# Kernel optimization log

Hardware: AMD Instinct MI355X
Metric: run time of the kernel (lower is better)

## Reference

```python
import jax, jax.numpy as jnp
import numpy as np

H = 512
W = 512
N_STROKES = 5000
S = 10          # samples_per_curve
K = 20          # strokes_per_pixel
CANVAS_COLOR = 0.5  # 'gray'
COARSE = 5      # coarse grid downsample factor (H//5, W//5)


def setup_inputs() -> dict:
    key = jax.random.key(0)
    ks = jax.random.split(key, 6)
    # stroke centers spread over the canvas
    location = jax.random.uniform(ks[0], (N_STROKES, 2), jnp.float32) * jnp.array([H, W], jnp.float32)
    # bezier control-point offsets relative to the stroke center
    curve_s = jax.random.normal(ks[1], (N_STROKES, 2), jnp.float32) * 8.0
    curve_e = jax.random.normal(ks[2], (N_STROKES, 2), jnp.float32) * 8.0
    curve_c = jax.random.normal(ks[3], (N_STROKES, 2), jnp.float32) * 8.0
    color = jax.random.uniform(ks[4], (N_STROKES, 3), jnp.float32)
    width = jax.random.uniform(ks[5], (N_STROKES, 1), jnp.float32) * 4.0 + 1.0
    return {"curve_s": curve_s, "curve_e": curve_e, "curve_c": curve_c,
            "color": color, "location": location, "width": width}


def _bezier_points(s, c, e, num_points):
    # s, c, e: [N, 2] -> [N, num_points, 2]
    t = jnp.linspace(0.0, 1.0, num_points).astype(jnp.float32)  # [S]
    omt2 = (1.0 - t) ** 2  # [S]
    t2 = t ** 2
    # x/y computed identically: c + (1-t)^2 (s - c) + t^2 (e - c)
    pts = c[:, None, :] + omt2[None, :, None] * (s - c)[:, None, :] \
          + t2[None, :, None] * (e - c)[:, None, :]
    return pts  # [N, S, 2]


def _nearest_upsample_idx(out_size, in_size):
    # torch F.interpolate mode='nearest': src = floor(dst * in/out)
    idx = jnp.floor(jnp.arange(out_size) * (in_size / out_size)).astype(jnp.int32)
    return jnp.clip(idx, 0, in_size - 1)


def reference(curve_s, curve_e, curve_c, color, location, width):
    # sample bezier curve points (absolute coords)
    pts = _bezier_points(curve_s + location, curve_c + location,
                         curve_e + location, S)  # [N, S, 2]

    # ---- coarse-grid KNN over stroke centers ----
    Hc, Wc = H // COARSE, W // COARSE
    tH = jnp.linspace(0.0, float(H), Hc).astype(jnp.float32)
    tW = jnp.linspace(0.0, float(W), Wc).astype(jnp.float32)
    Px, Py = jnp.meshgrid(tH, tW, indexing='ij')
    P = jnp.stack([Px, Py], axis=-1)  # [Hc, Wc, 2]
    D_centers = jnp.sum(jnp.square(P[:, :, None, :] - location), axis=-1)  # [Hc, Wc, N]
    _, idcs = jax.lax.top_k(-D_centers, K)  # [Hc, Wc, K]

    near_pts = pts[idcs]      # [Hc, Wc, K, S, 2]
    near_col = color[idcs]    # [Hc, Wc, K, 3]
    near_w = width[idcs]      # [Hc, Wc, K, 1]

    # ---- upsample coarse gathers to full res ----
    ih = _nearest_upsample_idx(H, Hc)
    iw = _nearest_upsample_idx(W, Wc)
    near_pts = near_pts[ih][:, iw]   # [H, W, K, S, 2] (nearest)
    near_col = near_col[ih][:, iw]   # [H, W, K, 3]   (nearest)
    # widths: bilinear (align_corners=False, no antialias) per channel
    near_w = jax.image.resize(near_w[..., 0], (H, W, K), method='linear')[..., None]  # [H, W, K, 1]

    # ---- full-res pixel grid ----
    tHf = jnp.linspace(0.0, float(H), H).astype(jnp.float32)
    tWf = jnp.linspace(0.0, float(W), W).astype(jnp.float32)
    Pxf, Pyf = jnp.meshgrid(tHf, tWf, indexing='ij')
    P_full = jnp.stack([Pxf, Pyf], axis=-1)  # [H, W, 2]

    # ---- per-pixel closest point on each polyline segment ----
    a = near_pts[:, :, :, :S - 1, :]              # [H, W, K, S-1, 2]
    b_a = near_pts[:, :, :, 1:, :] - a            # segment direction
    pa = P_full[:, :, None, None, :] - a          # pixel - segment start
    t = jnp.sum(b_a * pa, axis=-1) / jnp.sum(jnp.square(b_a), axis=-1)
    t = jnp.clip(t, 0.0, 1.0)
    closest = a + t[..., None] * b_a
    dist = jnp.sum(jnp.square(P_full[:, :, None, None, :] - closest), axis=-1)  # [H, W, K, S-1]

    D = jnp.min(dist, axis=(-1, -2))  # [H, W]
    min_per_stroke = jnp.min(dist, axis=-1)  # [H, W, K]
    ranking = jax.nn.softmax(100000.0 * (1.0 / (1e-08 + min_per_stroke)), axis=-1)  # [H, W, K]

    I_colors = jnp.einsum('hwkf,hwk->hwf', near_col, ranking)  # [H, W, 3]
    bs = jnp.einsum('hwkf,hwk->hwf', near_w, ranking)          # [H, W, 1]
    bs_mask = jax.nn.sigmoid(bs - D[..., None])
    canvas = jnp.full_like(I_colors, CANVAS_COLOR)
    I = I_colors * bs_mask + (1.0 - bs_mask) * canvas
    return I
```

## Files before the change

kernel.cpp:

```cpp
#include <hip/hip_runtime.h>
#include <math.h>

#define NS 5000
#define SS 10
#define KK 20
#define HC 102
#define NBIN 32
#define BINW 16.0f
#define CAP 192

#define WAVE_SYNC() __asm__ volatile("s_waitcnt lgkmcnt(0)" ::: "memory")

__global__ void prep_kernel(const float* __restrict__ cs, const float* __restrict__ ce,
                            const float* __restrict__ cc, const float* __restrict__ loc,
                            float* __restrict__ pts, float* __restrict__ invs,
                            int* __restrict__ binCnt) {
    int i = blockIdx.x * 256 + threadIdx.x;
    if (i >= NS) return;
    float lx = loc[i*2+0], ly = loc[i*2+1];
    float sx = cs[i*2+0] + lx, sy = cs[i*2+1] + ly;
    float ex = ce[i*2+0] + lx, ey = ce[i*2+1] + ly;
    float px = cc[i*2+0] + lx, py = cc[i*2+1] + ly;
    float qx[SS], qy[SS];
    #pragma unroll
    for (int j = 0; j < SS; ++j) {
        float t = (float)j * (1.0f / 9.0f);
        float omt = 1.0f - t;
        float omt2 = omt * omt, t2 = t * t;
        qx[j] = px + omt2 * (sx - px) + t2 * (ex - px);
        qy[j] = py + omt2 * (sy - py) + t2 * (ey - py);
        pts[(i*SS+j)*2+0] = qx[j];
        pts[(i*SS+j)*2+1] = qy[j];
    }
    #pragma unroll
    for (int sg = 0; sg < 9; ++sg) {
        float bx = qx[sg+1] - qx[sg], by = qy[sg+1] - qy[sg];
        invs[i*12+sg] = 1.0f / (bx*bx + by*by);
    }
    invs[i*12+9] = 0.0f; invs[i*12+10] = 0.0f; invs[i*12+11] = 0.0f;
    int b0 = min(max((int)(lx * (1.0f/BINW)), 0), NBIN-1);
    int b1 = min(max((int)(ly * (1.0f/BINW)), 0), NBIN-1);
    atomicAdd(&binCnt[b0*NBIN + b1], 1);
}

__global__ void binscan_kernel(const int* __restrict__ binCnt, int* __restrict__ binStart) {
    __shared__ int tmp[NBIN*NBIN];
    int t = threadIdx.x;
    tmp[t] = binCnt[t];
    __syncthreads();
    for (int off = 1; off < NBIN*NBIN; off <<= 1) {
        int v = (t >= off) ? tmp[t - off] : 0;
        __syncthreads();
        tmp[t] += v;
        __syncthreads();
    }
    binStart[t + 1] = tmp[t];
    if (t == 0) binStart[0] = 0;
}

__global__ void binscatter_kernel(const float* __restrict__ loc, const int* __restrict__ binStart,
                                  int* __restrict__ binFill, float2* __restrict__ sxy,
                                  int* __restrict__ sid) {
    int i = blockIdx.x * 256 + threadIdx.x;
    if (i >= NS) return;
    float l0 = loc[i*2+0], l1 = loc[i*2+1];
    int b0 = min(max((int)(l0 * (1.0f/BINW)), 0), NBIN-1);
    int b1 = min(max((int)(l1 * (1.0f/BINW)), 0), NBIN-1);
    int b = b0*NBIN + b1;
    int pos = binStart[b] + atomicAdd(&binFill[b], 1);
    sxy[pos] = make_float2(l0, l1);
    sid[pos] = i;
}

__global__ void __launch_bounds__(256) topk_kernel(const float* __restrict__ loc,
                                                   const float* __restrict__ width,
                                                   const float2* __restrict__ sxy,
                                                   const int* __restrict__ sid,
                                                   const int* __restrict__ binStart,
                                                   int* __restrict__ idcs,
                                                   float* __restrict__ wk) {
    __shared__ unsigned long long sk[4][CAP];
    int w = threadIdx.x >> 6, lane = threadIdx.x & 63;
    int cell = blockIdx.x * 4 + w;
    int ci = cell / HC, cj = cell - ci * HC;
    const float dc = 512.0f / 101.0f;
    float c0 = (float)ci * dc;
    float c1 = (float)cj * dc;
    unsigned long long below = (1ull << lane) - 1ull;

    float R = 30.0f;
    int cnt = 0;
    for (int attempt = 0; attempt < 5; ++attempt) {
        float R2 = R * R;
        int base = 0;
        int by0 = max((int)((c0 - R) * (1.0f/BINW)), 0);
        int by1 = min((int)((c0 + R) * (1.0f/BINW)), NBIN-1);
        int bx0 = max((int)((c1 - R) * (1.0f/BINW)), 0);
        int bx1 = min((int)((c1 + R) * (1.0f/BINW)), NBIN-1);
        for (int by = by0; by <= by1; ++by) {
            int s = binStart[by*NBIN + bx0];
            int e = binStart[by*NBIN + bx1 + 1];
            for (int t0 = s; t0 < e; t0 += 64) {
                int t = t0 + lane;
                int tc = min(t, e - 1);
                float2 p = sxy[tc];
                float dx = c0 - p.x, dy = c1 - p.y;
                float d = dx*dx + dy*dy;
                bool pred = (t < e) && (d < R2);
                unsigned long long mask = __ballot(pred);
                int pos = base + __popcll(mask & below);
                if (pred && pos < CAP)
                    sk[w][pos] = ((unsigned long long)__float_as_uint(d) << 32)
                               | (unsigned int)sid[tc];
                base += __popcll(mask);
            }
        }
        cnt = base;
        if (cnt >= KK) break;
        R *= 1.6f;
    }
    WAVE_SYNC();

    if (cnt >= KK && cnt <= CAP) {
        if (cnt <= 64) {
            unsigned long long k0 = (lane < cnt) ? sk[w][lane] : ~0ull;
            int r0 = 0;
            int j = 0;
            #pragma unroll 1
            for (; j + 4 <= cnt; j += 4) {
                unsigned long long a = sk[w][j],   b = sk[w][j+1];
                unsigned long long c = sk[w][j+2], d = sk[w][j+3];
                r0 += (int)(a < k0) + (int)(b < k0) + (int)(c < k0) + (int)(d < k0);
            }
            for (; j < cnt; ++j) r0 += (int)(sk[w][j] < k0);
            if (r0 < KK && lane < cnt) {
                int idx = (int)(unsigned int)(k0 & 0xffffffffull);
                idcs[cell*KK + r0] = idx;
                wk[cell*KK + r0]   = width[idx];
            }
        } else {
            unsigned long long k0 = (lane       < cnt) ? sk[w][lane]       : ~0ull;
            unsigned long long k1 = (lane + 64  < cnt) ? sk[w][lane + 64]  : ~0ull;
            unsigned long long k2 = (lane + 128 < cnt) ? sk[w][lane + 128] : ~0ull;
            int r0 = 0, r1 = 0, r2 = 0;
            #pragma unroll 1
            for (int j = 0; j < cnt; ++j) {
                unsigned long long a = sk[w][j];
                r0 += (int)(a < k0); r1 += (int)(a < k1); r2 += (int)(a < k2);
            }
            if (r0 < KK && lane < cnt) {
                int idx = (int)(unsigned int)(k0 & 0xffffffffull);
                idcs[cell*KK + r0] = idx;  wk[cell*KK + r0] = width[idx];
            }
            if (r1 < KK && lane + 64 < cnt) {
                int idx = (int)(unsigned int)(k1 & 0xffffffffull);
                idcs[cell*KK + r1] = idx;  wk[cell*KK + r1] = width[idx];
            }
            if (r2 < KK && lane + 128 < cnt) {
                int idx = (int)(unsigned int)(k2 & 0xffffffffull);
                idcs[cell*KK + r2] = idx;  wk[cell*KK + r2] = width[idx];
            }
        }
    } else {
        if (lane == 0) {
            float bd[KK]; int bi[KK];
            for (int k = 0; k < KK; ++k) { bd[k] = 3.4e38f; bi[k] = 0; }
            for (int n = 0; n < NS; ++n) {
                float dx = c0 - loc[n*2+0];
                float dy = c1 - loc[n*2+1];
                float d = dx*dx + dy*dy;
                if (d < bd[KK-1]) {
                    int p = KK - 1;
                    while (p > 0 && bd[p-1] > d) { bd[p] = bd[p-1]; bi[p] = bi[p-1]; --p; }
                    bd[p] = d; bi[p] = n;
                }
            }
            for (int k = 0; k < KK; ++k) {
                idcs[cell*KK + k] = bi[k];
                wk[cell*KK + k]   = width[bi[k]];
            }
        }
    }
}

__global__ void __launch_bounds__(256) render_kernel(const float* __restrict__ pts,
                                                     const float* __restrict__ invs,
                                                     const float* __restrict__ color,
                                                     const int* __restrict__ idcs,
                                                     const float* __restrict__ wk,
                                                     float* __restrict__ out) {
    int x = blockIdx.x * 64 + threadIdx.x;
    int y = blockIdx.y * 4  + threadIdx.y;
    const float df = 512.0f / 511.0f;
    float p0 = (float)y * df;
    float p1 = (float)x * df;
    int cy = (y * 51) >> 8;
    int cx = (x * 51) >> 8;
    const int* mi = idcs + (cy * HC + cx) * KK;

    const float sc = 102.0f / 512.0f;
    float iny = ((float)y + 0.5f) * sc - 0.5f;
    float inx = ((float)x + 0.5f) * sc - 0.5f;
    float y0f = floorf(iny), x0f = floorf(inx);
    float fy = iny - y0f, fx = inx - x0f;
    int y0 = min(max((int)y0f, 0), HC - 1);
    int y1 = min(max((int)y0f + 1, 0), HC - 1);
    int x0 = min(max((int)x0f, 0), HC - 1);
    int x1 = min(max((int)x0f + 1, 0), HC - 1);
    const float* w00 = wk + (y0 * HC + x0) * KK;
    const float* w01 = wk + (y0 * HC + x1) * KK;
    const float* w10 = wk + (y1 * HC + x0) * KK;
    const float* w11 = wk + (y1 * HC + x1) * KK;

    float m = -INFINITY, s = 0.0f;
    float a0 = 0.0f, a1 = 0.0f, a2 = 0.0f, wa = 0.0f;
    float D = INFINITY;

    #pragma unroll 1
    for (int k = 0; k < KK; ++k) {
        int idx = mi[k];
        const float4* pf = (const float4*)(pts  + idx * 20);
        const float4* vf = (const float4*)(invs + idx * 12);
        float4 f0 = pf[0], f1 = pf[1], f2 = pf[2], f3 = pf[3], f4 = pf[4];
        float4 i0 = vf[0], i1 = vf[1], i2 = vf[2];
        float qx[10] = {f0.x, f0.z, f1.x, f1.z, f2.x, f2.z, f3.x, f3.z, f4.x, f4.z};
        float qy[10] = {f0.y, f0.w, f1.y, f1.w, f2.y, f2.w, f3.y, f3.w, f4.y, f4.w};
        float iv[9]  = {i0.x, i0.y, i0.z, i0.w, i1.x, i1.y, i1.z, i1.w, i2.x};
        float mink = INFINITY;
        #pragma unroll
        for (int sg = 0; sg < 9; ++sg) {
            float ax = qx[sg], ay = qy[sg];
            float bx = qx[sg+1] - ax, by = qy[sg+1] - ay;
            float pax = p0 - ax, pay = p1 - ay;
            float dot = bx * pax + by * pay;
            float t = dot * iv[sg];
            t = fminf(fmaxf(t, 0.0f), 1.0f);
            float ccx = ax + t * bx, ccy = ay + t * by;
            float ddx = p0 - ccx, ddy = p1 - ccy;
            float d = ddx * ddx + ddy * ddy;
            mink = fminf(mink, d);
        }
        D = fminf(D, mink);
        float xk = 100000.0f / (1e-8f + mink);
        float wkv = (1.0f - fy) * ((1.0f - fx) * w00[k] + fx * w01[k])
                  +          fy * ((1.0f - fx) * w10[k] + fx * w11[k]);
        float c0v = color[idx*3+0], c1v = color[idx*3+1], c2v = color[idx*3+2];
        if (xk > m) {
            float scl = __expf(m - xk);
            s  = s  * scl + 1.0f;
            a0 = a0 * scl + c0v;
            a1 = a1 * scl + c1v;
            a2 = a2 * scl + c2v;
            wa = wa * scl + wkv;
            m = xk;
        } else {
            float e = __expf(xk - m);
            s  += e;
            a0 += c0v * e;
            a1 += c1v * e;
            a2 += c2v * e;
            wa += wkv * e;
        }
    }
    float inv = 1.0f / s;
    float bs = wa * inv;
    float msk = 1.0f / (1.0f + __expf(-(bs - D)));
    float o0 = a0 * inv * msk + (1.0f - msk) * 0.5f;
    float o1 = a1 * inv * msk + (1.0f - msk) * 0.5f;
    float o2 = a2 * inv * msk + (1.0f - msk) * 0.5f;
    int base = (y * 512 + x) * 3;
    out[base+0] = o0;
    out[base+1] = o1;
    out[base+2] = o2;
}

extern "C" void kernel_launch(void* const* d_in, const int* in_sizes, int n_in,
                              void* d_out, int out_size, void* d_ws, size_t ws_size,
                              hipStream_t stream) {
    const float* cs    = (const float*)d_in[0];
    const float* ce    = (const float*)d_in[1];
    const float* cc    = (const float*)d_in[2];
    const float* color = (const float*)d_in[3];
    const float* loc   = (const float*)d_in[4];
    const float* width = (const float*)d_in[5];
    float* out = (float*)d_out;

    char* p = (char*)d_ws;
    float*  pts      = (float*)p;                 p += NS * SS * 2 * sizeof(float);
    float*  invs     = (float*)p;                 p += NS * 12 * sizeof(float);
    int*    idcs     = (int*)p;                   p += (size_t)HC*HC*KK*sizeof(int);
    float*  wk       = (float*)p;                 p += (size_t)HC*HC*KK*sizeof(float);
    int*    binCnt   = (int*)p;                   p += NBIN*NBIN*sizeof(int);
    int*    binFill  = (int*)p;                   p += NBIN*NBIN*sizeof(int);
    int*    binStart = (int*)p;                   p += 4112;
    float2* sxy      = (float2*)p;                p += NS * sizeof(float2);
    int*    sid      = (int*)p;

    hipMemsetAsync(binCnt, 0, 2 * NBIN * NBIN * sizeof(int), stream);

    prep_kernel      <<<(NS + 255) / 256, 256, 0, stream>>>(cs, ce, cc, loc, pts, invs, binCnt);
    binscan_kernel   <<<1, NBIN*NBIN, 0, stream>>>(binCnt, binStart);
    binscatter_kernel<<<(NS + 255) / 256, 256, 0, stream>>>(loc, binStart, binFill, sxy, sid);
    topk_kernel      <<<(HC*HC)/4, 256, 0, stream>>>(loc, width, sxy, sid, binStart, idcs, wk);
    render_kernel    <<<dim3(512/64, 512/4), dim3(64, 4), 0, stream>>>(pts, invs, color, idcs, wk, out);
}
```

Measured before the change: 135.7 us.

## Pack stroke data into 128B records, branchless softmax, shuffle-based bin scan

Stroke points and inverse segment lengths are merged into one 32-float record per stroke, and color plus width go into a float4 table, so render fetches each stroke with fewer, aligned loads. The render loop preloads all K indices as int4 vectors, unrolls by 4 and uses a branchless online-softmax update, with launch bounds raised for occupancy. The bin prefix scan is rewritten with wave shuffles over 256 threads. Costs: two exps per stroke instead of one, more register pressure from unrolling, and an extra color/width gather in prep.

After: 134.5 us. About the same (-0.9%).

```diff
diff --git a/kernel.cpp b/kernel.cpp
--- a/kernel.cpp
+++ b/kernel.cpp
@@ -13,7 +13,8 @@
 
 __global__ void prep_kernel(const float* __restrict__ cs, const float* __restrict__ ce,
                             const float* __restrict__ cc, const float* __restrict__ loc,
-                            float* __restrict__ pts, float* __restrict__ invs,
+                            const float* __restrict__ color, const float* __restrict__ width,
+                            float* __restrict__ sdata, float4* __restrict__ ctab,
                             int* __restrict__ binCnt) {
     int i = blockIdx.x * 256 + threadIdx.x;
     if (i >= NS) return;
@@ -29,32 +30,43 @@
         float omt2 = omt * omt, t2 = t * t;
         qx[j] = px + omt2 * (sx - px) + t2 * (ex - px);
         qy[j] = py + omt2 * (sy - py) + t2 * (ey - py);
-        pts[(i*SS+j)*2+0] = qx[j];
-        pts[(i*SS+j)*2+1] = qy[j];
+        sdata[i*32 + 2*j + 0] = qx[j];
+        sdata[i*32 + 2*j + 1] = qy[j];
     }
     #pragma unroll
     for (int sg = 0; sg < 9; ++sg) {
         float bx = qx[sg+1] - qx[sg], by = qy[sg+1] - qy[sg];
-        invs[i*12+sg] = 1.0f / (bx*bx + by*by);
-    }
-    invs[i*12+9] = 0.0f; invs[i*12+10] = 0.0f; invs[i*12+11] = 0.0f;
+        sdata[i*32 + 20 + sg] = 1.0f / (bx*bx + by*by);
+    }
+    sdata[i*32 + 29] = 0.0f; sdata[i*32 + 30] = 0.0f; sdata[i*32 + 31] = 0.0f;
+    ctab[i] = make_float4(color[i*3+0], color[i*3+1], color[i*3+2], width[i]);
     int b0 = min(max((int)(lx * (1.0f/BINW)), 0), NBIN-1);
     int b1 = min(max((int)(ly * (1.0f/BINW)), 0), NBIN-1);
     atomicAdd(&binCnt[b0*NBIN + b1], 1);
 }
 
 __global__ void binscan_kernel(const int* __restrict__ binCnt, int* __restrict__ binStart) {
-    __shared__ int tmp[NBIN*NBIN];
+    __shared__ int wsum[4];
     int t = threadIdx.x;
-    tmp[t] = binCnt[t];
+    int lane = t & 63, w = t >> 6;
+    int4 v = ((const int4*)binCnt)[t];
+    int s0 = v.x, s1 = s0 + v.y, s2 = s1 + v.z, s3 = s2 + v.w;
+    int x = s3;
+    #pragma unroll
+    for (int off = 1; off < 64; off <<= 1) {
+        int y = __shfl_up(x, off, 64);
+        if (lane >= off) x += y;
+    }
+    if (lane == 63) wsum[w] = x;
     __syncthreads();
-    for (int off = 1; off < NBIN*NBIN; off <<= 1) {
-        int v = (t >= off) ? tmp[t - off] : 0;
-        __syncthreads();
-        tmp[t] += v;
-        __syncthreads();
-    }
-    binStart[t + 1] = tmp[t];
+    int woff = 0;
+    #pragma unroll
+    for (int i = 0; i < 4; ++i) woff += (i < w) ? wsum[i] : 0;
+    int texcl = woff + x - s3;
+    binStart[4*t+1] = texcl + s0;
+    binStart[4*t+2] = texcl + s1;
+    binStart[4*t+3] = texcl + s2;
+    binStart[4*t+4] = texcl + s3;
     if (t == 0) binStart[0] = 0;
 }
 
@@ -183,12 +195,11 @@
     }
 }
 
-__global__ void __launch_bounds__(256) render_kernel(const float* __restrict__ pts,
-                                                     const float* __restrict__ invs,
-                                                     const float* __restrict__ color,
-                                                     const int* __restrict__ idcs,
-                                                     const float* __restrict__ wk,
-                                                     float* __restrict__ out) {
+__global__ void __launch_bounds__(256, 4) render_kernel(const float* __restrict__ sdata,
+                                                        const float4* __restrict__ ctab,
+                                                        const int* __restrict__ idcs,
+                                                        const float* __restrict__ wk,
+                                                        float* __restrict__ out) {
     int x = blockIdx.x * 64 + threadIdx.x;
     int y = blockIdx.y * 4  + threadIdx.y;
     const float df = 512.0f / 511.0f;
@@ -196,7 +207,11 @@
     float p1 = (float)x * df;
     int cy = (y * 51) >> 8;
     int cx = (x * 51) >> 8;
-    const int* mi = idcs + (cy * HC + cx) * KK;
+
+    const int4* mip = (const int4*)(idcs + (cy * HC + cx) * KK);
+    int4 m0 = mip[0], m1 = mip[1], m2 = mip[2], m3 = mip[3], m4 = mip[4];
+    int idxs[KK] = {m0.x,m0.y,m0.z,m0.w, m1.x,m1.y,m1.z,m1.w, m2.x,m2.y,m2.z,m2.w,
+                    m3.x,m3.y,m3.z,m3.w, m4.x,m4.y,m4.z,m4.w};
 
     const float sc = 102.0f / 512.0f;
     float iny = ((float)y + 0.5f) * sc - 0.5f;
@@ -216,13 +231,13 @@
     float a0 = 0.0f, a1 = 0.0f, a2 = 0.0f, wa = 0.0f;
     float D = INFINITY;
 
-    #pragma unroll 1
+    #pragma unroll 4
     for (int k = 0; k < KK; ++k) {
-        int idx = mi[k];
-        const float4* pf = (const float4*)(pts  + idx * 20);
-        const float4* vf = (const float4*)(invs + idx * 12);
-        float4 f0 = pf[0], f1 = pf[1], f2 = pf[2], f3 = pf[3], f4 = pf[4];
-        float4 i0 = vf[0], i1 = vf[1], i2 = vf[2];
+        int idx = idxs[k];
+        const float4* sp = (const float4*)(sdata + idx * 32);
+        float4 f0 = sp[0], f1 = sp[1], f2 = sp[2], f3 = sp[3], f4 = sp[4];
+        float4 i0 = sp[5], i1 = sp[6], i2 = sp[7];
+        float4 cw = ctab[idx];
         float qx[10] = {f0.x, f0.z, f1.x, f1.z, f2.x, f2.z, f3.x, f3.z, f4.x, f4.z};
         float qy[10] = {f0.y, f0.w, f1.y, f1.w, f2.y, f2.w, f3.y, f3.w, f4.y, f4.w};
         float iv[9]  = {i0.x, i0.y, i0.z, i0.w, i1.x, i1.y, i1.z, i1.w, i2.x};
@@ -241,26 +256,18 @@
             mink = fminf(mink, d);
         }
         D = fminf(D, mink);
-        float xk = 100000.0f / (1e-8f + mink);
+        float z = 100000.0f / (1e-8f + mink);
         float wkv = (1.0f - fy) * ((1.0f - fx) * w00[k] + fx * w01[k])
                   +          fy * ((1.0f - fx) * w10[k] + fx * w11[k]);
-        float c0v = color[idx*3+0], c1v = color[idx*3+1], c2v = color[idx*3+2];
-        if (xk > m) {
-            float scl = __expf(m - xk);
-            s  = s  * scl + 1.0f;
-            a0 = a0 * scl + c0v;
-            a1 = a1 * scl + c1v;
-            a2 = a2 * scl + c2v;
-            wa = wa * scl + wkv;
-            m = xk;
-        } else {
-            float e = __expf(xk - m);
-            s  += e;
-            a0 += c0v * e;
-            a1 += c1v * e;
-            a2 += c2v * e;
-            wa += wkv * e;
-        }
+        float nm  = fmaxf(m, z);
+        float scl = __expf(m - nm);
+        float e   = __expf(z - nm);
+        s  = s  * scl + e;
+        a0 = a0 * scl + cw.x * e;
+        a1 = a1 * scl + cw.y * e;
+        a2 = a2 * scl + cw.z * e;
+        wa = wa * scl + wkv  * e;
+        m = nm;
     }
     float inv = 1.0f / s;
     float bs = wa * inv;
@@ -286,8 +293,8 @@
     float* out = (float*)d_out;
 
     char* p = (char*)d_ws;
-    float*  pts      = (float*)p;                 p += NS * SS * 2 * sizeof(float);
-    float*  invs     = (float*)p;                 p += NS * 12 * sizeof(float);
+    float*  sdata    = (float*)p;                 p += NS * 32 * sizeof(float);
+    float4* ctab     = (float4*)p;                p += NS * sizeof(float4);
     int*    idcs     = (int*)p;                   p += (size_t)HC*HC*KK*sizeof(int);
     float*  wk       = (float*)p;                 p += (size_t)HC*HC*KK*sizeof(float);
     int*    binCnt   = (int*)p;                   p += NBIN*NBIN*sizeof(int);
@@ -298,9 +305,10 @@
 
     hipMemsetAsync(binCnt, 0, 2 * NBIN * NBIN * sizeof(int), stream);
 
-    prep_kernel      <<<(NS + 255) / 256, 256, 0, stream>>>(cs, ce, cc, loc, pts, invs, binCnt);
-    binscan_kernel   <<<1, NBIN*NBIN, 0, stream>>>(binCnt, binStart);
+    prep_kernel      <<<(NS + 255) / 256, 256, 0, stream>>>(cs, ce, cc, loc, color, width,
+                                                            sdata, ctab, binCnt);
+    binscan_kernel   <<<1, 256, 0, stream>>>(binCnt, binStart);
     binscatter_kernel<<<(NS + 255) / 256, 256, 0, stream>>>(loc, binStart, binFill, sxy, sid);
     topk_kernel      <<<(HC*HC)/4, 256, 0, stream>>>(loc, width, sxy, sid, binStart, idcs, wk);
-    render_kernel    <<<dim3(512/64, 512/4), dim3(64, 4), 0, stream>>>(pts, invs, color, idcs, wk, out);
-}
+    render_kernel    <<<dim3(512/64, 512/4), dim3(64, 4), 0, stream>>>(sdata, ctab, idcs, wk, out);
+}
```
